# Kernel optimization log

Measured on AMD Instinct MI355X. Metric: run time of the kernel, lower is better.

Reference implementation:

```python
import jax, jax.numpy as jnp
import numpy as np

N, IN_DIM = 50000, 1024
E = 100000
NUM_REL = 40
HEADS, OUT_DIM = 4, 200
HID = HEADS * OUT_DIM  # 800
B = 8192
NEG_SLOPE = 0.2


def setup_inputs() -> dict:
    key = jax.random.key(0)
    ks = jax.random.split(key, 12)
    node_emb = jax.random.normal(ks[0], (N, IN_DIM), dtype=jnp.float32)
    # RelGAT learnable params
    W = jax.random.normal(ks[1], (IN_DIM, HID), dtype=jnp.float32) * (1.0 / np.sqrt(IN_DIM))
    bias = jnp.zeros((HID,), dtype=jnp.float32)
    a_src = jax.random.normal(ks[2], (HEADS, OUT_DIM), dtype=jnp.float32) * 0.1
    a_dst = jax.random.normal(ks[3], (HEADS, OUT_DIM), dtype=jnp.float32) * 0.1
    a_rel = jax.random.normal(ks[4], (HEADS, OUT_DIM), dtype=jnp.float32) * 0.1
    rel_feat = jax.random.normal(ks[5], (NUM_REL, HID), dtype=jnp.float32) * 0.1
    # DistMult scorer relation embeddings
    rel_emb = jax.random.normal(ks[6], (NUM_REL, HID), dtype=jnp.float32) * 0.1
    # Graph structure (constants)
    edge_index = jax.random.randint(ks[7], (2, E), 0, N, dtype=jnp.int64)
    edge_type = jax.random.randint(ks[8], (E,), 0, NUM_REL, dtype=jnp.int64)
    # Triple batch
    src_ids = jax.random.randint(ks[9], (B,), 0, N, dtype=jnp.int64)
    rel_ids = jax.random.randint(ks[10], (B,), 0, NUM_REL, dtype=jnp.int64)
    dst_ids = jax.random.randint(ks[11], (B,), 0, N, dtype=jnp.int64)
    return dict(node_emb=node_emb, W=W, bias=bias, a_src=a_src, a_dst=a_dst,
                a_rel=a_rel, rel_feat=rel_feat, rel_emb=rel_emb,
                edge_index=edge_index, edge_type=edge_type,
                src_ids=src_ids, rel_ids=rel_ids, dst_ids=dst_ids)


def _rel_gat(node_emb, W, bias, a_src, a_dst, a_rel, rel_feat, edge_index, edge_type):
    src, dst = edge_index[0], edge_index[1]
    h = (node_emb @ W).reshape(N, HEADS, OUT_DIM)          # [N,H,D]
    hs = h[src]                                            # [E,H,D] gather
    hd = h[dst]                                            # [E,H,D] gather
    r = rel_feat[edge_type].reshape(E, HEADS, OUT_DIM)     # [E,H,D]
    # relation-conditioned attention logits per head
    logits = (jnp.einsum('ehd,hd->eh', hs, a_src)
              + jnp.einsum('ehd,hd->eh', hd, a_dst)
              + jnp.einsum('ehd,hd->eh', r, a_rel))        # [E,H]
    logits = jax.nn.leaky_relu(logits, NEG_SLOPE)
    # segment softmax over incoming edges of each destination node
    seg_max = jax.ops.segment_max(logits, dst, num_segments=N)   # [N,H]
    e = jnp.exp(logits - seg_max[dst])                           # [E,H]
    denom = jax.ops.segment_sum(e, dst, num_segments=N)          # [N,H]
    alpha = e / denom[dst]                                       # [E,H]
    # weighted scatter-aggregate of source messages
    out = jax.ops.segment_sum(alpha[:, :, None] * hs, dst, num_segments=N)  # [N,H,D]
    return out.reshape(N, HID) + bias                            # dropout: eval mode (identity)


def reference(node_emb, W, bias, a_src, a_dst, a_rel, rel_feat, rel_emb,
              edge_index, edge_type, src_ids, rel_ids, dst_ids):
    refined = _rel_gat(node_emb, W, bias, a_src, a_dst, a_rel, rel_feat,
                       edge_index, edge_type)                # [N, HID]
    src_vec = refined[src_ids]                               # [B, HID]
    dst_vec = refined[dst_ids]                               # [B, HID]
    # DistMult: sum(s * r * d)
    scores = jnp.sum(src_vec * rel_emb[rel_ids] * dst_vec, axis=-1)  # [B]
    return scores
```

## Files before the change

kernel.cpp:

```cpp
#include <hip/hip_runtime.h>
#include <hip/hip_bf16.h>
#include <math.h>

#define NN 50000
#define IN_DIM 1024
#define EE 100000
#define NUM_REL 40
#define HEADS 4
#define OUT_D 200
#define HID 800
#define BB 8192
#define SLOT_CAP 16384
#define SRC_CAP 50176

typedef __attribute__((ext_vector_type(8))) short short8;
typedef __attribute__((ext_vector_type(4))) float f32x4;

__device__ inline unsigned short f2bf(float f) {
    unsigned int u = __float_as_uint(f);
    u += 0x7FFF + ((u >> 16) & 1);
    return (unsigned short)(u >> 16);
}
__device__ inline float bf2f(unsigned short s) {
    return __uint_as_float(((unsigned int)s) << 16);
}

__global__ void k_init(int* slot_of_node, int* srcslot_of_node, int* deg, int* counters) {
    int i = blockIdx.x * 256 + threadIdx.x;
    if (i < NN) { slot_of_node[i] = -1; srcslot_of_node[i] = -1; }
    if (i < SLOT_CAP) deg[i] = 0;
    if (i < 4) counters[i] = 0;
}

__global__ void k_build_slots(const int* src_ids, const int* dst_ids,
                              int* slot_of_node, int* counters) {
    int i = blockIdx.x * 256 + threadIdx.x;
    if (i >= 2 * BB) return;
    int n = (i < BB) ? src_ids[i] : dst_ids[i - BB];
    if (slot_of_node[n] == -1) {
        if (atomicCAS(&slot_of_node[n], -1, -2) == -1) {
            int s = atomicAdd(&counters[0], 1);
            slot_of_node[n] = s;
        }
    }
}

__global__ void k_wa(const float* W, const float* a_src, const float* a_dst,
                     const float* a_rel, const float* rel_feat,
                     float* Wa, float* prel) {
    int tid = blockIdx.x * 256 + threadIdx.x;
    if (tid < IN_DIM * 8) {
        int k = tid >> 3, c = tid & 7;
        const float* a = (c < 4) ? a_src : a_dst;
        int h = c & 3;
        float s = 0.f;
        for (int d = 0; d < OUT_D; ++d)
            s += W[k * HID + h * OUT_D + d] * a[h * OUT_D + d];
        Wa[k * 8 + c] = s;
    } else if (tid < IN_DIM * 8 + NUM_REL * HEADS) {
        int j = tid - IN_DIM * 8;
        int r = j >> 2, h = j & 3;
        float s = 0.f;
        for (int d = 0; d < OUT_D; ++d)
            s += rel_feat[r * HID + h * OUT_D + d] * a_rel[h * OUT_D + d];
        prel[j] = s;
    }
}

__global__ __launch_bounds__(256) void k_sgemm(const float* x, const float* Wa,
                                               float* sS, float* sD) {
    __shared__ float swa[IN_DIM * 9];
    for (int i = threadIdx.x; i < IN_DIM * 8; i += 256)
        swa[(i >> 3) * 9 + (i & 7)] = Wa[i];
    __syncthreads();
    int w = threadIdx.x >> 6, lane = threadIdx.x & 63;
    int n = blockIdx.x * 4 + w;
    if (n >= NN) return;
    float acc[8] = {};
    const float* xr = x + (size_t)n * IN_DIM;
    for (int j = 0; j < 16; ++j) {
        int k = j * 64 + lane;
        float xv = xr[k];
        const float* wr = &swa[k * 9];
#pragma unroll
        for (int c = 0; c < 8; ++c) acc[c] += xv * wr[c];
    }
#pragma unroll
    for (int c = 0; c < 8; ++c)
        for (int off = 32; off; off >>= 1) acc[c] += __shfl_down(acc[c], off, 64);
    if (lane == 0) {
#pragma unroll
        for (int h = 0; h < 4; ++h) {
            sS[n * 4 + h] = acc[h];
            sD[n * 4 + h] = acc[4 + h];
        }
    }
}

__global__ void k_edge1(const int* ei, const int* etype, const int* slot_of_node,
                        int* srcslot_of_node, int* node_of_srcslot, int* counters,
                        const float* sS, const float* sD, const float* prel,
                        float* logit_buf, int* deg) {
    int e = blockIdx.x * 256 + threadIdx.x;
    if (e >= EE) return;
    int dn = ei[EE + e];
    int slot = slot_of_node[dn];
    if (slot < 0) return;
    int sn = ei[e];
    if (srcslot_of_node[sn] == -1) {
        if (atomicCAS(&srcslot_of_node[sn], -1, -2) == -1) {
            int t = atomicAdd(&counters[1], 1);
            node_of_srcslot[t] = sn;
            srcslot_of_node[sn] = t;
        }
    }
    int r = etype[e];
#pragma unroll
    for (int h = 0; h < 4; ++h) {
        float lg = sS[sn * 4 + h] + sD[dn * 4 + h] + prel[r * 4 + h];
        lg = lg > 0.f ? lg : 0.2f * lg;
        logit_buf[e * 4 + h] = lg;
    }
    atomicAdd(&deg[slot], 1);
}

__global__ __launch_bounds__(256) void k_scan(const int* deg, int* base, int* cursor) {
    __shared__ int pref[257];
    int t = threadIdx.x;
    int s = 0;
    for (int i = 0; i < SLOT_CAP / 256; ++i) s += deg[t * (SLOT_CAP / 256) + i];
    pref[t + 1] = s;
    if (t == 0) pref[0] = 0;
    __syncthreads();
    if (t == 0)
        for (int i = 1; i <= 256; ++i) pref[i] += pref[i - 1];
    __syncthreads();
    int r = pref[t];
    for (int i = 0; i < SLOT_CAP / 256; ++i) {
        int idx = t * (SLOT_CAP / 256) + i;
        base[idx] = r;
        cursor[idx] = r;
        r += deg[idx];
    }
}

__global__ void k_place(const int* ei, const int* slot_of_node, const int* srcslot_of_node,
                        int* cursor, int* edge_id, int* tlist) {
    int e = blockIdx.x * 256 + threadIdx.x;
    if (e >= EE) return;
    int dn = ei[EE + e];
    int slot = slot_of_node[dn];
    if (slot < 0) return;
    int pos = atomicAdd(&cursor[slot], 1);
    edge_id[pos] = e;
    tlist[pos] = srcslot_of_node[ei[e]];
}

__global__ void k_gather_cast(const float* x, const int* node_of_srcslot,
                              const int* counters, unsigned short* xg) {
    int gid = blockIdx.x * 256 + threadIdx.x;
    int row = gid >> 7;
    if (row >= counters[1]) return;
    int j = (gid & 127) * 8;
    int node = node_of_srcslot[row];
    const float* src = x + (size_t)node * IN_DIM + j;
    float4 a = *(const float4*)(src);
    float4 b = *(const float4*)(src + 4);
    unsigned short o[8] = {f2bf(a.x), f2bf(a.y), f2bf(a.z), f2bf(a.w),
                           f2bf(b.x), f2bf(b.y), f2bf(b.z), f2bf(b.w)};
    *(short8*)(xg + (size_t)row * IN_DIM + j) = *(short8*)o;
}

__global__ __launch_bounds__(256) void k_wt(const float* W, unsigned short* Wt) {
    __shared__ float tile[64][65];
    int k0 = blockIdx.x * 64, c0 = blockIdx.y * 64;
    int t = threadIdx.x;
    {
        int kk = t >> 2, cc = (t & 3) * 16;
        for (int i = 0; i < 16; ++i) {
            int c = c0 + cc + i;
            tile[cc + i][kk] = (c < HID) ? W[(size_t)(k0 + kk) * HID + c] : 0.f;
        }
    }
    __syncthreads();
    {
        int cc = t >> 2, kk = (t & 3) * 16;
        unsigned short o[16];
        for (int i = 0; i < 16; ++i) o[i] = f2bf(tile[cc][kk + i]);
        *(short8*)(Wt + (size_t)(c0 + cc) * IN_DIM + k0 + kk) = *(short8*)o;
        *(short8*)(Wt + (size_t)(c0 + cc) * IN_DIM + k0 + kk + 8) = *(short8*)(o + 8);
    }
}

#define GBM 128
#define GBN 128
#define GBK 32
#define LSTR 40
__global__ __launch_bounds__(256) void k_hgemm(const unsigned short* xg, const unsigned short* Wt,
                                               const int* counters, unsigned short* h_src) {
    int nsrc = counters[1];
    int row0 = blockIdx.y * GBM;
    if (row0 >= nsrc) return;
    int col0 = blockIdx.x * GBN;
    __shared__ unsigned short As[GBM * LSTR];
    __shared__ unsigned short Bs[GBN * LSTR];
    int t = threadIdx.x;
    int srow = t >> 1, soff = (t & 1) * 16;
    const unsigned short* ag = xg + (size_t)(row0 + srow) * IN_DIM + soff;
    const unsigned short* bg = Wt + (size_t)(col0 + srow) * IN_DIM + soff;
    int w = t >> 6, lane = t & 63;
    int wr = (w >> 1) * 64, wc = (w & 1) * 64;
    int fm = lane & 15, fq = lane >> 4;
    f32x4 acc[4][4] = {};
    for (int k0 = 0; k0 < IN_DIM; k0 += GBK) {
        short8 av0 = *(const short8*)(ag + k0);
        short8 av1 = *(const short8*)(ag + k0 + 8);
        short8 bv0 = *(const short8*)(bg + k0);
        short8 bv1 = *(const short8*)(bg + k0 + 8);
        __syncthreads();
        *(short8*)&As[srow * LSTR + soff] = av0;
        *(short8*)&As[srow * LSTR + soff + 8] = av1;
        *(short8*)&Bs[srow * LSTR + soff] = bv0;
        *(short8*)&Bs[srow * LSTR + soff + 8] = bv1;
        __syncthreads();
        short8 af[4], bf[4];
#pragma unroll
        for (int i = 0; i < 4; ++i)
            af[i] = *(const short8*)&As[(wr + i * 16 + fm) * LSTR + fq * 8];
#pragma unroll
        for (int j = 0; j < 4; ++j)
            bf[j] = *(const short8*)&Bs[(wc + j * 16 + fm) * LSTR + fq * 8];
#pragma unroll
        for (int i = 0; i < 4; ++i)
#pragma unroll
            for (int j = 0; j < 4; ++j)
                acc[i][j] = __builtin_amdgcn_mfma_f32_16x16x32_bf16(af[i], bf[j], acc[i][j], 0, 0, 0);
    }
#pragma unroll
    for (int i = 0; i < 4; ++i) {
#pragma unroll
        for (int j = 0; j < 4; ++j) {
            int gcol = col0 + wc + j * 16 + fm;
            if (gcol >= HID) continue;
#pragma unroll
            for (int r = 0; r < 4; ++r) {
                int grow = row0 + wr + i * 16 + fq * 4 + r;
                if (grow < nsrc)
                    h_src[(size_t)grow * HID + gcol] = f2bf(acc[i][j][r]);
            }
        }
    }
}

__global__ __launch_bounds__(256) void k_aggregate(const int* counters, const int* base,
                                                   const int* deg, const int* edge_id,
                                                   const int* tlist, const float* logit_buf,
                                                   const unsigned short* h_src, const float* bias,
                                                   float* refined) {
    int b = blockIdx.x;
    if (b >= counters[0]) return;
    int beg = base[b], d = deg[b];
    __shared__ float m4[4], den4[4];
    __shared__ float alpha[64][4];
    __shared__ int tsl[64];
    int t = threadIdx.x;
    if (t < 4) {
        float m = -3e38f;
        for (int j = 0; j < d; ++j)
            m = fmaxf(m, logit_buf[edge_id[beg + j] * 4 + t]);
        float s = 0.f;
        for (int j = 0; j < d; ++j)
            s += expf(logit_buf[edge_id[beg + j] * 4 + t] - m);
        m4[t] = m;
        den4[t] = s;
    }
    __syncthreads();
    int h0 = t / 200, h1 = (t + 256) / 200, h2 = (t + 512) / 200;
    float acc0 = 0.f, acc1 = 0.f, acc2 = 0.f, acc3 = 0.f;
    for (int j0 = 0; j0 < d; j0 += 64) {
        int nc = min(64, d - j0);
        if (t < nc * 4) {
            int j = t >> 2, h = t & 3;
            int e = edge_id[beg + j0 + j];
            alpha[j][h] = expf(logit_buf[e * 4 + h] - m4[h]) / den4[h];
            if (h == 0) tsl[j] = tlist[beg + j0 + j];
        }
        __syncthreads();
        for (int j = 0; j < nc; ++j) {
            const unsigned short* hr = h_src + (size_t)tsl[j] * HID;
            acc0 += alpha[j][h0] * bf2f(hr[t]);
            acc1 += alpha[j][h1] * bf2f(hr[t + 256]);
            acc2 += alpha[j][h2] * bf2f(hr[t + 512]);
            if (t < 32) acc3 += alpha[j][3] * bf2f(hr[768 + t]);
        }
        __syncthreads();
    }
    float* rr = refined + (size_t)b * HID;
    rr[t] = acc0 + bias[t];
    rr[t + 256] = acc1 + bias[t + 256];
    rr[t + 512] = acc2 + bias[t + 512];
    if (t < 32) rr[768 + t] = acc3 + bias[768 + t];
}

__global__ __launch_bounds__(256) void k_score(const int* src_ids, const int* rel_ids,
                                               const int* dst_ids, const int* slot_of_node,
                                               const float* rel_emb, const float* refined,
                                               float* out) {
    int gid = blockIdx.x * 256 + threadIdx.x;
    int b = gid >> 6;
    int lane = threadIdx.x & 63;
    if (b >= BB) return;
    int ss = slot_of_node[src_ids[b]];
    int ds = slot_of_node[dst_ids[b]];
    int r = rel_ids[b];
    const float* sv = refined + (size_t)ss * HID;
    const float* dv = refined + (size_t)ds * HID;
    const float* rv = rel_emb + (size_t)r * HID;
    float acc = 0.f;
    for (int c = lane; c < HID; c += 64) acc += sv[c] * rv[c] * dv[c];
    for (int off = 32; off; off >>= 1) acc += __shfl_down(acc, off, 64);
    if (lane == 0) out[b] = acc;
}

extern "C" void kernel_launch(void* const* d_in, const int* in_sizes, int n_in,
                              void* d_out, int out_size, void* d_ws, size_t ws_size,
                              hipStream_t stream) {
    const float* node_emb = (const float*)d_in[0];
    const float* W        = (const float*)d_in[1];
    const float* bias     = (const float*)d_in[2];
    const float* a_src    = (const float*)d_in[3];
    const float* a_dst    = (const float*)d_in[4];
    const float* a_rel    = (const float*)d_in[5];
    const float* rel_feat = (const float*)d_in[6];
    const float* rel_emb  = (const float*)d_in[7];
    const int* edge_index = (const int*)d_in[8];
    const int* edge_type  = (const int*)d_in[9];
    const int* src_ids    = (const int*)d_in[10];
    const int* rel_ids    = (const int*)d_in[11];
    const int* dst_ids    = (const int*)d_in[12];
    float* out = (float*)d_out;

    char* w = (char*)d_ws;
    auto alloc = [&](size_t bytes) -> void* {
        void* p = (void*)w;
        w += (bytes + 255) & ~(size_t)255;
        return p;
    };
    int* slot_of_node    = (int*)alloc((size_t)NN * 4);
    int* srcslot_of_node = (int*)alloc((size_t)NN * 4);
    int* node_of_srcslot = (int*)alloc((size_t)NN * 4);
    int* counters        = (int*)alloc(256);
    int* deg             = (int*)alloc((size_t)SLOT_CAP * 4);
    int* base            = (int*)alloc((size_t)SLOT_CAP * 4);
    int* cursor          = (int*)alloc((size_t)SLOT_CAP * 4);
    int* edge_id         = (int*)alloc((size_t)EE * 4);
    int* tlist           = (int*)alloc((size_t)EE * 4);
    float* sS        = (float*)alloc((size_t)NN * 4 * 4);
    float* sD        = (float*)alloc((size_t)NN * 4 * 4);
    float* Wa        = (float*)alloc((size_t)IN_DIM * 8 * 4);
    float* prel      = (float*)alloc((size_t)NUM_REL * 4 * 4);
    float* logit_buf = (float*)alloc((size_t)EE * 4 * 4);
    unsigned short* xg    = (unsigned short*)alloc((size_t)SRC_CAP * IN_DIM * 2);
    unsigned short* Wt    = (unsigned short*)alloc((size_t)896 * IN_DIM * 2);
    unsigned short* h_src = (unsigned short*)alloc((size_t)NN * HID * 2);
    float* refined = (float*)alloc((size_t)SLOT_CAP * HID * 4);

    k_init<<<256, 256, 0, stream>>>(slot_of_node, srcslot_of_node, deg, counters);
    k_build_slots<<<(2 * BB + 255) / 256, 256, 0, stream>>>(src_ids, dst_ids, slot_of_node, counters);
    k_wa<<<(IN_DIM * 8 + NUM_REL * HEADS + 255) / 256, 256, 0, stream>>>(
        W, a_src, a_dst, a_rel, rel_feat, Wa, prel);
    k_sgemm<<<(NN + 3) / 4, 256, 0, stream>>>(node_emb, Wa, sS, sD);
    k_edge1<<<(EE + 255) / 256, 256, 0, stream>>>(edge_index, edge_type, slot_of_node,
                                                  srcslot_of_node, node_of_srcslot, counters,
                                                  sS, sD, prel, logit_buf, deg);
    k_scan<<<1, 256, 0, stream>>>(deg, base, cursor);
    k_place<<<(EE + 255) / 256, 256, 0, stream>>>(edge_index, slot_of_node, srcslot_of_node,
                                                  cursor, edge_id, tlist);
    k_gather_cast<<<(NN * 128 + 255) / 256, 256, 0, stream>>>(node_emb, node_of_srcslot,
                                                              counters, xg);
    k_wt<<<dim3(IN_DIM / 64, 896 / 64), 256, 0, stream>>>(W, Wt);
    dim3 ggrid((HID + GBN - 1) / GBN, (NN + GBM - 1) / GBM);
    k_hgemm<<<ggrid, 256, 0, stream>>>(xg, Wt, counters, h_src);
    k_aggregate<<<SLOT_CAP, 256, 0, stream>>>(counters, base, deg, edge_id, tlist,
                                              logit_buf, h_src, bias, refined);
    k_score<<<(BB * 64 + 255) / 256, 256, 0, stream>>>(src_ids, rel_ids, dst_ids,
                                                       slot_of_node, rel_emb, refined, out);
}
```

Before: 539.8 us.

## Compute attention scores only for needed nodes and fuse gather-cast into score pass

The per-node attention-score GEMV now runs only over nodes that appear as batch endpoints or as sources of relevant edges, collected in a 'need' list, instead of all 50k nodes. The same pass writes the bf16 copy of each source row, replacing the separate gather-cast kernel. Logits are computed in edge placement order, so aggregation reads them contiguously without an edge-id indirection. The bf16 GEMM now loads tiles directly from global memory into LDS, and the scoring kernel reads float4 vectors. The risks are atomic contention on the new need counter and LDS bank conflicts in the unpadded tile layout.

Result: slower. 612.1 us (+13.4%).

```diff
diff --git a/kernel.cpp b/kernel.cpp
--- a/kernel.cpp
+++ b/kernel.cpp
@@ -24,6 +24,11 @@
 __device__ inline float bf2f(unsigned short s) {
     return __uint_as_float(((unsigned int)s) << 16);
 }
+__device__ inline void gl2lds16(const unsigned short* g, unsigned short* l) {
+    __builtin_amdgcn_global_load_lds(
+        (const __attribute__((address_space(1))) void*)g,
+        (__attribute__((address_space(3))) void*)l, 16, 0, 0);
+}
 
 __global__ void k_init(int* slot_of_node, int* srcslot_of_node, int* deg, int* counters) {
     int i = blockIdx.x * 256 + threadIdx.x;
@@ -33,7 +38,7 @@
 }
 
 __global__ void k_build_slots(const int* src_ids, const int* dst_ids,
-                              int* slot_of_node, int* counters) {
+                              int* slot_of_node, int* counters, int* need) {
     int i = blockIdx.x * 256 + threadIdx.x;
     if (i >= 2 * BB) return;
     int n = (i < BB) ? src_ids[i] : dst_ids[i - BB];
@@ -41,6 +46,8 @@
         if (atomicCAS(&slot_of_node[n], -1, -2) == -1) {
             int s = atomicAdd(&counters[0], 1);
             slot_of_node[n] = s;
+            int q = atomicAdd(&counters[2], 1);
+            need[q] = n;
         }
     }
 }
@@ -67,40 +74,8 @@
     }
 }
 
-__global__ __launch_bounds__(256) void k_sgemm(const float* x, const float* Wa,
-                                               float* sS, float* sD) {
-    __shared__ float swa[IN_DIM * 9];
-    for (int i = threadIdx.x; i < IN_DIM * 8; i += 256)
-        swa[(i >> 3) * 9 + (i & 7)] = Wa[i];
-    __syncthreads();
-    int w = threadIdx.x >> 6, lane = threadIdx.x & 63;
-    int n = blockIdx.x * 4 + w;
-    if (n >= NN) return;
-    float acc[8] = {};
-    const float* xr = x + (size_t)n * IN_DIM;
-    for (int j = 0; j < 16; ++j) {
-        int k = j * 64 + lane;
-        float xv = xr[k];
-        const float* wr = &swa[k * 9];
-#pragma unroll
-        for (int c = 0; c < 8; ++c) acc[c] += xv * wr[c];
-    }
-#pragma unroll
-    for (int c = 0; c < 8; ++c)
-        for (int off = 32; off; off >>= 1) acc[c] += __shfl_down(acc[c], off, 64);
-    if (lane == 0) {
-#pragma unroll
-        for (int h = 0; h < 4; ++h) {
-            sS[n * 4 + h] = acc[h];
-            sD[n * 4 + h] = acc[4 + h];
-        }
-    }
-}
-
-__global__ void k_edge1(const int* ei, const int* etype, const int* slot_of_node,
-                        int* srcslot_of_node, int* node_of_srcslot, int* counters,
-                        const float* sS, const float* sD, const float* prel,
-                        float* logit_buf, int* deg) {
+__global__ void k_edge0(const int* ei, const int* slot_of_node,
+                        int* srcslot_of_node, int* counters, int* need, int* deg) {
     int e = blockIdx.x * 256 + threadIdx.x;
     if (e >= EE) return;
     int dn = ei[EE + e];
@@ -110,16 +85,12 @@
     if (srcslot_of_node[sn] == -1) {
         if (atomicCAS(&srcslot_of_node[sn], -1, -2) == -1) {
             int t = atomicAdd(&counters[1], 1);
-            node_of_srcslot[t] = sn;
             srcslot_of_node[sn] = t;
-        }
-    }
-    int r = etype[e];
-#pragma unroll
-    for (int h = 0; h < 4; ++h) {
-        float lg = sS[sn * 4 + h] + sD[dn * 4 + h] + prel[r * 4 + h];
-        lg = lg > 0.f ? lg : 0.2f * lg;
-        logit_buf[e * 4 + h] = lg;
+            if (slot_of_node[sn] < 0) {
+                int q = atomicAdd(&counters[2], 1);
+                need[q] = sn;
+            }
+        }
     }
     atomicAdd(&deg[slot], 1);
 }
@@ -144,31 +115,64 @@
     }
 }
 
-__global__ void k_place(const int* ei, const int* slot_of_node, const int* srcslot_of_node,
-                        int* cursor, int* edge_id, int* tlist) {
+__global__ __launch_bounds__(256) void k_sgemm(const float* x, const float* Wa,
+                                               const int* need, const int* counters,
+                                               const int* srcslot_of_node,
+                                               float* sS, float* sD, unsigned short* xg) {
+    if (blockIdx.x * 4 >= counters[2]) return;
+    __shared__ float swa[IN_DIM * 9];
+    for (int i = threadIdx.x; i < IN_DIM * 8; i += 256)
+        swa[(i >> 3) * 9 + (i & 7)] = Wa[i];
+    __syncthreads();
+    int w = threadIdx.x >> 6, lane = threadIdx.x & 63;
+    int idx = blockIdx.x * 4 + w;
+    if (idx >= counters[2]) return;
+    int n = need[idx];
+    int ts = srcslot_of_node[n];
+    float acc[8] = {};
+    const float* xr = x + (size_t)n * IN_DIM;
+    unsigned short* xo = xg + (size_t)(ts < 0 ? 0 : ts) * IN_DIM;
+    for (int j = 0; j < 16; ++j) {
+        int k = j * 64 + lane;
+        float xv = xr[k];
+        if (ts >= 0) xo[k] = f2bf(xv);
+        const float* wr = &swa[k * 9];
+#pragma unroll
+        for (int c = 0; c < 8; ++c) acc[c] += xv * wr[c];
+    }
+#pragma unroll
+    for (int c = 0; c < 8; ++c)
+        for (int off = 32; off; off >>= 1) acc[c] += __shfl_down(acc[c], off, 64);
+    if (lane == 0) {
+#pragma unroll
+        for (int h = 0; h < 4; ++h) {
+            sS[n * 4 + h] = acc[h];
+            sD[n * 4 + h] = acc[4 + h];
+        }
+    }
+}
+
+__global__ void k_place(const int* ei, const int* etype, const int* slot_of_node,
+                        const int* srcslot_of_node, int* cursor,
+                        const float* sS, const float* sD, const float* prel,
+                        float* clogit, int* tlist) {
     int e = blockIdx.x * 256 + threadIdx.x;
     if (e >= EE) return;
     int dn = ei[EE + e];
     int slot = slot_of_node[dn];
     if (slot < 0) return;
+    int sn = ei[e];
+    int r = etype[e];
     int pos = atomicAdd(&cursor[slot], 1);
-    edge_id[pos] = e;
-    tlist[pos] = srcslot_of_node[ei[e]];
-}
-
-__global__ void k_gather_cast(const float* x, const int* node_of_srcslot,
-                              const int* counters, unsigned short* xg) {
-    int gid = blockIdx.x * 256 + threadIdx.x;
-    int row = gid >> 7;
-    if (row >= counters[1]) return;
-    int j = (gid & 127) * 8;
-    int node = node_of_srcslot[row];
-    const float* src = x + (size_t)node * IN_DIM + j;
-    float4 a = *(const float4*)(src);
-    float4 b = *(const float4*)(src + 4);
-    unsigned short o[8] = {f2bf(a.x), f2bf(a.y), f2bf(a.z), f2bf(a.w),
-                           f2bf(b.x), f2bf(b.y), f2bf(b.z), f2bf(b.w)};
-    *(short8*)(xg + (size_t)row * IN_DIM + j) = *(short8*)o;
+    tlist[pos] = srcslot_of_node[sn];
+    float4 lg;
+    float* lp = (float*)&lg;
+#pragma unroll
+    for (int h = 0; h < 4; ++h) {
+        float v = sS[sn * 4 + h] + sD[dn * 4 + h] + prel[r * 4 + h];
+        lp[h] = v > 0.f ? v : 0.2f * v;
+    }
+    *(float4*)&clogit[(size_t)pos * 4] = lg;
 }
 
 __global__ __launch_bounds__(256) void k_wt(const float* W, unsigned short* Wt) {
@@ -195,41 +199,43 @@
 #define GBM 128
 #define GBN 128
 #define GBK 32
-#define LSTR 40
 __global__ __launch_bounds__(256) void k_hgemm(const unsigned short* xg, const unsigned short* Wt,
                                                const int* counters, unsigned short* h_src) {
     int nsrc = counters[1];
     int row0 = blockIdx.y * GBM;
     if (row0 >= nsrc) return;
     int col0 = blockIdx.x * GBN;
-    __shared__ unsigned short As[GBM * LSTR];
-    __shared__ unsigned short Bs[GBN * LSTR];
+    __shared__ unsigned short As[GBM * GBK];
+    __shared__ unsigned short Bs[GBN * GBK];
     int t = threadIdx.x;
-    int srow = t >> 1, soff = (t & 1) * 16;
-    const unsigned short* ag = xg + (size_t)(row0 + srow) * IN_DIM + soff;
-    const unsigned short* bg = Wt + (size_t)(col0 + srow) * IN_DIM + soff;
+    int sg = t >> 6, sfq = (t >> 4) & 3, sfm = t & 15;
+    const unsigned short* a0 = xg + (size_t)(row0 + sg * 16 + sfm) * IN_DIM + sfq * 8;
+    const unsigned short* a1 = a0 + (size_t)64 * IN_DIM;
+    const unsigned short* b0 = Wt + (size_t)(col0 + sg * 16 + sfm) * IN_DIM + sfq * 8;
+    const unsigned short* b1 = b0 + (size_t)64 * IN_DIM;
+    unsigned short* la0 = As + t * 8;
+    unsigned short* la1 = As + (256 + t) * 8;
+    unsigned short* lb0 = Bs + t * 8;
+    unsigned short* lb1 = Bs + (256 + t) * 8;
     int w = t >> 6, lane = t & 63;
+    int ga = (w >> 1) * 4, gb = (w & 1) * 4;
     int wr = (w >> 1) * 64, wc = (w & 1) * 64;
     int fm = lane & 15, fq = lane >> 4;
     f32x4 acc[4][4] = {};
     for (int k0 = 0; k0 < IN_DIM; k0 += GBK) {
-        short8 av0 = *(const short8*)(ag + k0);
-        short8 av1 = *(const short8*)(ag + k0 + 8);
-        short8 bv0 = *(const short8*)(bg + k0);
-        short8 bv1 = *(const short8*)(bg + k0 + 8);
         __syncthreads();
-        *(short8*)&As[srow * LSTR + soff] = av0;
-        *(short8*)&As[srow * LSTR + soff + 8] = av1;
-        *(short8*)&Bs[srow * LSTR + soff] = bv0;
-        *(short8*)&Bs[srow * LSTR + soff + 8] = bv1;
+        gl2lds16(a0 + k0, la0);
+        gl2lds16(a1 + k0, la1);
+        gl2lds16(b0 + k0, lb0);
+        gl2lds16(b1 + k0, lb1);
         __syncthreads();
         short8 af[4], bf[4];
 #pragma unroll
         for (int i = 0; i < 4; ++i)
-            af[i] = *(const short8*)&As[(wr + i * 16 + fm) * LSTR + fq * 8];
+            af[i] = *(const short8*)&As[((ga + i) * 64 + lane) * 8];
 #pragma unroll
         for (int j = 0; j < 4; ++j)
-            bf[j] = *(const short8*)&Bs[(wc + j * 16 + fm) * LSTR + fq * 8];
+            bf[j] = *(const short8*)&Bs[((gb + j) * 64 + lane) * 8];
 #pragma unroll
         for (int i = 0; i < 4; ++i)
 #pragma unroll
@@ -253,8 +259,8 @@
 }
 
 __global__ __launch_bounds__(256) void k_aggregate(const int* counters, const int* base,
-                                                   const int* deg, const int* edge_id,
-                                                   const int* tlist, const float* logit_buf,
+                                                   const int* deg, const int* tlist,
+                                                   const float* clogit,
                                                    const unsigned short* h_src, const float* bias,
                                                    float* refined) {
     int b = blockIdx.x;
@@ -267,10 +273,10 @@
     if (t < 4) {
         float m = -3e38f;
         for (int j = 0; j < d; ++j)
-            m = fmaxf(m, logit_buf[edge_id[beg + j] * 4 + t]);
+            m = fmaxf(m, clogit[(size_t)(beg + j) * 4 + t]);
         float s = 0.f;
         for (int j = 0; j < d; ++j)
-            s += expf(logit_buf[edge_id[beg + j] * 4 + t] - m);
+            s += expf(clogit[(size_t)(beg + j) * 4 + t] - m);
         m4[t] = m;
         den4[t] = s;
     }
@@ -281,8 +287,7 @@
         int nc = min(64, d - j0);
         if (t < nc * 4) {
             int j = t >> 2, h = t & 3;
-            int e = edge_id[beg + j0 + j];
-            alpha[j][h] = expf(logit_buf[e * 4 + h] - m4[h]) / den4[h];
+            alpha[j][h] = expf(clogit[(size_t)(beg + j0 + j) * 4 + h] - m4[h]) / den4[h];
             if (h == 0) tsl[j] = tlist[beg + j0 + j];
         }
         __syncthreads();
@@ -317,7 +322,12 @@
     const float* dv = refined + (size_t)ds * HID;
     const float* rv = rel_emb + (size_t)r * HID;
     float acc = 0.f;
-    for (int c = lane; c < HID; c += 64) acc += sv[c] * rv[c] * dv[c];
+    for (int c4 = lane; c4 < 200; c4 += 64) {
+        float4 s = *(const float4*)(sv + c4 * 4);
+        float4 dq = *(const float4*)(dv + c4 * 4);
+        float4 rr = *(const float4*)(rv + c4 * 4);
+        acc += s.x * rr.x * dq.x + s.y * rr.y * dq.y + s.z * rr.z * dq.z + s.w * rr.w * dq.w;
+    }
     for (int off = 32; off; off >>= 1) acc += __shfl_down(acc, off, 64);
     if (lane == 0) out[b] = acc;
 }
@@ -348,41 +358,40 @@
     };
     int* slot_of_node    = (int*)alloc((size_t)NN * 4);
     int* srcslot_of_node = (int*)alloc((size_t)NN * 4);
-    int* node_of_srcslot = (int*)alloc((size_t)NN * 4);
+    int* need            = (int*)alloc((size_t)NN * 4);
     int* counters        = (int*)alloc(256);
     int* deg             = (int*)alloc((size_t)SLOT_CAP * 4);
     int* base            = (int*)alloc((size_t)SLOT_CAP * 4);
     int* cursor          = (int*)alloc((size_t)SLOT_CAP * 4);
-    int* edge_id         = (int*)alloc((size_t)EE * 4);
     int* tlist           = (int*)alloc((size_t)EE * 4);
+    float* clogit    = (float*)alloc((size_t)EE * 4 * 4);
     float* sS        = (float*)alloc((size_t)NN * 4 * 4);
     float* sD        = (float*)alloc((size_t)NN * 4 * 4);
     float* Wa        = (float*)alloc((size_t)IN_DIM * 8 * 4);
     float* prel      = (float*)alloc((size_t)NUM_REL * 4 * 4);
-    float* logit_buf = (float*)alloc((size_t)EE * 4 * 4);
     unsigned short* xg    = (unsigned short*)alloc((size_t)SRC_CAP * IN_DIM * 2);
     unsigned short* Wt    = (unsigned short*)alloc((size_t)896 * IN_DIM * 2);
     unsigned short* h_src = (unsigned short*)alloc((size_t)NN * HID * 2);
     float* refined = (float*)alloc((size_t)SLOT_CAP * HID * 4);
 
     k_init<<<256, 256, 0, stream>>>(slot_of_node, srcslot_of_node, deg, counters);
-    k_build_slots<<<(2 * BB + 255) / 256, 256, 0, stream>>>(src_ids, dst_ids, slot_of_node, counters);
+    k_build_slots<<<(2 * BB + 255) / 256, 256, 0, stream>>>(src_ids, dst_ids, slot_of_node,
+                                                            counters, need);
     k_wa<<<(IN_DIM * 8 + NUM_REL * HEADS + 255) / 256, 256, 0, stream>>>(
         W, a_src, a_dst, a_rel, rel_feat, Wa, prel);
-    k_sgemm<<<(NN + 3) / 4, 256, 0, stream>>>(node_emb, Wa, sS, sD);
-    k_edge1<<<(EE + 255) / 256, 256, 0, stream>>>(edge_index, edge_type, slot_of_node,
-                                                  srcslot_of_node, node_of_srcslot, counters,
-                                                  sS, sD, prel, logit_buf, deg);
+    k_edge0<<<(EE + 255) / 256, 256, 0, stream>>>(edge_index, slot_of_node,
+                                                  srcslot_of_node, counters, need, deg);
     k_scan<<<1, 256, 0, stream>>>(deg, base, cursor);
-    k_place<<<(EE + 255) / 256, 256, 0, stream>>>(edge_index, slot_of_node, srcslot_of_node,
-                                                  cursor, edge_id, tlist);
-    k_gather_cast<<<(NN * 128 + 255) / 256, 256, 0, stream>>>(node_emb, node_of_srcslot,
-                                                              counters, xg);
+    k_sgemm<<<(NN + 3) / 4, 256, 0, stream>>>(node_emb, Wa, need, counters,
+                                              srcslot_of_node, sS, sD, xg);
     k_wt<<<dim3(IN_DIM / 64, 896 / 64), 256, 0, stream>>>(W, Wt);
+    k_place<<<(EE + 255) / 256, 256, 0, stream>>>(edge_index, edge_type, slot_of_node,
+                                                  srcslot_of_node, cursor, sS, sD, prel,
+                                                  clogit, tlist);
     dim3 ggrid((HID + GBN - 1) / GBN, (NN + GBM - 1) / GBM);
     k_hgemm<<<ggrid, 256, 0, stream>>>(xg, Wt, counters, h_src);
-    k_aggregate<<<SLOT_CAP, 256, 0, stream>>>(counters, base, deg, edge_id, tlist,
-                                              logit_buf, h_src, bias, refined);
+    k_aggregate<<<SLOT_CAP, 256, 0, stream>>>(counters, base, deg, tlist,
+                                              clogit, h_src, bias, refined);
     k_score<<<(BB * 64 + 255) / 256, 256, 0, stream>>>(src_ids, rel_ids, dst_ids,
                                                        slot_of_node, rel_emb, refined, out);
 }
```
